# Kernel tuning notes

Measured on AMD Instinct MI355X. Metric: run time of the kernel, lower is better.

Reference implementation:

```python
import jax, jax.numpy as jnp
import numpy as np

B, T, S, E, H, V = 64, 32, 64, 128, 256, 32000


def setup_inputs() -> dict:
    key = jax.random.key(0)
    ks = jax.random.split(key, 13)
    n = lambda k, sh, s=1.0: jax.random.normal(k, sh, dtype=jnp.float32) * s
    return {
        "target": n(ks[0], (B, T, E)),
        "inp": n(ks[1], (B, T, E)),
        "pos_feature": n(ks[2], (B, E)),
        "encoder_state": n(ks[3], (B, H)),
        "encoder_output": n(ks[4], (B, S, 2 * H)),
        "W_ih": n(ks[5], (3 * H, 3 * E + H), 0.05),
        "W_hh": n(ks[6], (3 * H, H), 0.05),
        "b_ih": n(ks[7], (3 * H,), 0.05),
        "b_hh": n(ks[8], (3 * H,), 0.05),
        "Win_w": n(ks[9], (2 * H, H), 0.05),
        "Win_b": n(ks[10], (2 * H,), 0.05),
        "Wout_w": n(ks[11], (V, 3 * H), 0.05),
        "Wout_b": n(ks[12], (V,), 0.05),
    }


def reference(target, inp, pos_feature, encoder_state, encoder_output,
              W_ih, W_hh, b_ih, b_hh, Win_w, Win_b, Wout_w, Wout_b):
    bsz = target.shape[0]
    hdim = W_hh.shape[1]

    def gru_cell(x, h):
        gi = x @ W_ih.T + b_ih          # [B, 3H]
        gh = h @ W_hh.T + b_hh          # [B, 3H]
        i_r, i_z, i_n = jnp.split(gi, 3, axis=1)
        h_r, h_z, h_n = jnp.split(gh, 3, axis=1)
        r = jax.nn.sigmoid(i_r + h_r)
        z = jax.nn.sigmoid(i_z + h_z)
        n = jnp.tanh(i_n + r * h_n)
        return (1.0 - z) * n + z * h

    def step(hs, xs):
        dec_in, in_t = xs                                   # [B,E], [B,E]
        x = jnp.concatenate([dec_in, pos_feature, encoder_state, in_t], axis=1)
        hs = gru_cell(x, hs)
        q = hs @ Win_w.T + Win_b                            # [B, 2H]
        attn = jnp.einsum('bsd,bd->bs', encoder_output, q)  # [B, S]
        score = jax.nn.softmax(attn, axis=1)
        h_star = jnp.einsum('bs,bsd->bd', score, encoder_output)  # [B, 2H]
        feat = jnp.concatenate([h_star, hs], axis=1)        # [B, 3H]
        out = jax.nn.log_softmax(jax.nn.relu(feat @ Wout_w.T + Wout_b), axis=1)
        return hs, out

    hs0 = jnp.zeros((bsz, hdim), dtype=target.dtype)
    xs = (jnp.swapaxes(target, 0, 1), jnp.swapaxes(inp, 0, 1))  # time-major
    hs, outputs = jax.lax.scan(step, hs0, xs)
    return hs, outputs  # hs: [B,H], outputs: [T,B,V]
```

## Files before the change

kernel.cpp:

```cpp
#include <hip/hip_runtime.h>
#include <hip/hip_bf16.h>


typedef __attribute__((ext_vector_type(8))) short  s8v;
typedef __attribute__((ext_vector_type(8))) __bf16 bf8v;
typedef __attribute__((ext_vector_type(4))) float  f4v;
typedef __attribute__((ext_vector_type(2))) float  f2v;

#define DEV static __device__ __forceinline__

DEV ushort f2b(float f) {
  unsigned u = __float_as_uint(f);
  u += 0x7fffu + ((u >> 16) & 1u);
  return (ushort)(u >> 16);
}
DEV float b2fs(short s) { return __uint_as_float(((unsigned)(ushort)s) << 16); }

__global__ __launch_bounds__(256) void k_gather(
    const float* __restrict__ target, const float* __restrict__ inp,
    const float* __restrict__ posf,   const float* __restrict__ encs,
    ushort* __restrict__ X) {
  int tb = blockIdx.x; int t = tb >> 6, b = tb & 63;
  size_t xrow = (size_t)tb * 640;
  for (int c = threadIdx.x; c < 640; c += 256) {
    float v;
    if (c < 128)      v = target[((size_t)b * 32 + t) * 128 + c];
    else if (c < 256) v = posf[(size_t)b * 128 + (c - 128)];
    else if (c < 512) v = encs[(size_t)b * 256 + (c - 256)];
    else              v = inp[((size_t)b * 32 + t) * 128 + (c - 512)];
    X[xrow + c] = f2b(v);
  }
}

template <bool RELU>
__global__ __launch_bounds__(256) void k_gemm_bt(
    const ushort* __restrict__ A, const float* __restrict__ B,
    const float* __restrict__ bias, float* __restrict__ Out,
    int N, int K) {
  __shared__ __align__(16) ushort As[128 * 40];
  __shared__ __align__(16) ushort Bs[128 * 40];
  const int m0 = blockIdx.x * 128, n0 = blockIdx.y * 128;
  const int tid = threadIdx.x;
  const int lane = tid & 63, wv = tid >> 6;
  const int wm = (wv >> 1) * 64, wn = (wv & 1) * 64;
  const int fr = lane & 15, fq = lane >> 4;
  const int srow = tid >> 2, scol = (tid & 3) * 8;
  f4v acc[4][4];
#pragma unroll
  for (int i = 0; i < 4; ++i)
#pragma unroll
    for (int j = 0; j < 4; ++j) acc[i][j] = {0.f, 0.f, 0.f, 0.f};
  const ushort* ag = A + (size_t)(m0 + srow) * K + scol;
  const float*  bg = B + (size_t)(n0 + srow) * K + scol;
  for (int k0 = 0; k0 < K; k0 += 32) {
    s8v a0 = *(const s8v*)(ag + k0);
    s8v a1 = *(const s8v*)(ag + k0 + (size_t)64 * K);
    f4v b00 = *(const f4v*)(bg + k0);
    f4v b01 = *(const f4v*)(bg + k0 + 4);
    f4v b10 = *(const f4v*)(bg + k0 + (size_t)64 * K);
    f4v b11 = *(const f4v*)(bg + k0 + (size_t)64 * K + 4);
    s8v b0, b1;
#pragma unroll
    for (int u = 0; u < 4; ++u) {
      b0[u]     = (short)f2b(b00[u]);
      b0[u + 4] = (short)f2b(b01[u]);
      b1[u]     = (short)f2b(b10[u]);
      b1[u + 4] = (short)f2b(b11[u]);
    }
    __syncthreads();
    *(s8v*)&As[srow * 40 + scol] = a0;
    *(s8v*)&As[(srow + 64) * 40 + scol] = a1;
    *(s8v*)&Bs[srow * 40 + scol] = b0;
    *(s8v*)&Bs[(srow + 64) * 40 + scol] = b1;
    __syncthreads();
    bf8v af[4], bfr[4];
#pragma unroll
    for (int i = 0; i < 4; ++i)
      af[i] = *(const bf8v*)&As[(wm + i * 16 + fr) * 40 + fq * 8];
#pragma unroll
    for (int j = 0; j < 4; ++j)
      bfr[j] = *(const bf8v*)&Bs[(wn + j * 16 + fr) * 40 + fq * 8];
#pragma unroll
    for (int i = 0; i < 4; ++i)
#pragma unroll
      for (int j = 0; j < 4; ++j)
        acc[i][j] = __builtin_amdgcn_mfma_f32_16x16x32_bf16(af[i], bfr[j],
                                                            acc[i][j], 0, 0, 0);
  }
  float bj[4];
#pragma unroll
  for (int j = 0; j < 4; ++j) bj[j] = bias[n0 + wn + j * 16 + fr];
#pragma unroll
  for (int i = 0; i < 4; ++i) {
#pragma unroll
    for (int j = 0; j < 4; ++j) {
#pragma unroll
      for (int r = 0; r < 4; ++r) {
        int gm = m0 + wm + i * 16 + fq * 4 + r;
        int gn = n0 + wn + j * 16 + fr;
        float v = acc[i][j][r] + bj[j];
        if (RELU) v = fmaxf(v, 0.f);
        Out[(size_t)gm * N + gn] = v;
      }
    }
  }
}

__global__ __launch_bounds__(256) void k_recur(
    const float* __restrict__ gi_all,
    const float* __restrict__ eo,
    const float* __restrict__ Whh,
    const float* __restrict__ bhh,
    const float* __restrict__ Winw,
    const float* __restrict__ Winb,
    ushort* __restrict__ feat,
    float* __restrict__ hs_out) {
  const int b = blockIdx.x, t = threadIdx.x;
  __shared__ __align__(16) float h[256];
  __shared__ __align__(16) float q[512];
  __shared__ float attnp[64][4];
  __shared__ float score[64];
  const float* eoB = eo + (size_t)b * 32768;
  const float bhr = bhh[t], bhz = bhh[t + 256], bhn = bhh[t + 512];
  const float qb0 = Winb[t], qb1 = Winb[t + 256];
  const float* wr = Whh + t * 256;
  const float* wz = Whh + (t + 256) * 256;
  const float* wn = Whh + (t + 512) * 256;
  const float* w0 = Winw + t * 256;
  const float* w1 = Winw + (t + 256) * 256;
  h[t] = 0.f;
  __syncthreads();
  for (int st = 0; st < 32; ++st) {
    const float* gi = gi_all + ((size_t)st * 64 + b) * 768;
    float ar = bhr, az = bhz, an = bhn;
#pragma unroll 4
    for (int k = 0; k < 256; k += 8) {
      f4v ha = *(const f4v*)&h[k];
      f4v hb = *(const f4v*)&h[k + 4];
      f4v r0 = *(const f4v*)(wr + k), r1 = *(const f4v*)(wr + k + 4);
      f4v z0 = *(const f4v*)(wz + k), z1 = *(const f4v*)(wz + k + 4);
      f4v n0 = *(const f4v*)(wn + k), n1 = *(const f4v*)(wn + k + 4);
      float hv[8] = {ha.x, ha.y, ha.z, ha.w, hb.x, hb.y, hb.z, hb.w};
      float rv[8] = {r0.x, r0.y, r0.z, r0.w, r1.x, r1.y, r1.z, r1.w};
      float zv[8] = {z0.x, z0.y, z0.z, z0.w, z1.x, z1.y, z1.z, z1.w};
      float nv[8] = {n0.x, n0.y, n0.z, n0.w, n1.x, n1.y, n1.z, n1.w};
#pragma unroll
      for (int u = 0; u < 8; ++u) {
        ar = fmaf(hv[u], rv[u], ar);
        az = fmaf(hv[u], zv[u], az);
        an = fmaf(hv[u], nv[u], an);
      }
    }
    float r = 1.f / (1.f + __expf(-(gi[t] + ar)));
    float z = 1.f / (1.f + __expf(-(gi[t + 256] + az)));
    float e2 = __expf(2.f * (gi[t + 512] + r * an));
    float n = 1.f - 2.f / (e2 + 1.f);
    float hnew = (1.f - z) * n + z * h[t];
    __syncthreads();
    h[t] = hnew;
    __syncthreads();
    float a0 = qb0, a1 = qb1;
#pragma unroll 4
    for (int k = 0; k < 256; k += 8) {
      f4v ha = *(const f4v*)&h[k];
      f4v hb = *(const f4v*)&h[k + 4];
      f4v u00 = *(const f4v*)(w0 + k), u01 = *(const f4v*)(w0 + k + 4);
      f4v u10 = *(const f4v*)(w1 + k), u11 = *(const f4v*)(w1 + k + 4);
      float hv[8] = {ha.x, ha.y, ha.z, ha.w, hb.x, hb.y, hb.z, hb.w};
      float v0[8] = {u00.x, u00.y, u00.z, u00.w, u01.x, u01.y, u01.z, u01.w};
      float v1[8] = {u10.x, u10.y, u10.z, u10.w, u11.x, u11.y, u11.z, u11.w};
#pragma unroll
      for (int u = 0; u < 8; ++u) {
        a0 = fmaf(hv[u], v0[u], a0);
        a1 = fmaf(hv[u], v1[u], a1);
      }
    }
    q[t] = a0;
    q[t + 256] = a1;
    __syncthreads();
    {
      int s = t >> 2, p = t & 3;
      const float* ep = eoB + s * 512 + p * 128;
      const float* qp = &q[p * 128];
      float aa = 0.f;
#pragma unroll 4
      for (int dc = 0; dc < 128; dc += 8) {
        f4v e0 = *(const f4v*)(ep + dc), e1 = *(const f4v*)(ep + dc + 4);
        f4v q0 = *(const f4v*)(qp + dc), q1 = *(const f4v*)(qp + dc + 4);
        aa = fmaf(q0.x, e0.x, aa); aa = fmaf(q0.y, e0.y, aa);
        aa = fmaf(q0.z, e0.z, aa); aa = fmaf(q0.w, e0.w, aa);
        aa = fmaf(q1.x, e1.x, aa); aa = fmaf(q1.y, e1.y, aa);
        aa = fmaf(q1.z, e1.z, aa); aa = fmaf(q1.w, e1.w, aa);
      }
      attnp[s][p] = aa;
    }
    __syncthreads();
    if (t < 64) {
      float a = attnp[t][0] + attnp[t][1] + attnp[t][2] + attnp[t][3];
      float m = a;
#pragma unroll
      for (int off = 32; off > 0; off >>= 1) m = fmaxf(m, __shfl_xor(m, off));
      float e = __expf(a - m);
      float ss = e;
#pragma unroll
      for (int off = 32; off > 0; off >>= 1) ss += __shfl_xor(ss, off);
      score[t] = e / ss;
    }
    __syncthreads();
    {
      int d0 = 2 * t;
      float s0 = 0.f, s1 = 0.f;
#pragma unroll 8
      for (int s2 = 0; s2 < 64; ++s2) {
        float sc = score[s2];
        f2v ev = *(const f2v*)(eoB + s2 * 512 + d0);
        s0 = fmaf(sc, ev.x, s0);
        s1 = fmaf(sc, ev.y, s1);
      }
      size_t row = ((size_t)st * 64 + b) * 768;
      feat[row + d0] = f2b(s0);
      feat[row + d0 + 1] = f2b(s1);
      feat[row + 512 + t] = f2b(h[t]);
    }
    __syncthreads();
  }
  hs_out[(size_t)b * 256 + t] = h[t];
}

__global__ __launch_bounds__(256) void k_logsm(float* __restrict__ out) {
  float* p = out + (size_t)blockIdx.x * 32000;
  const int t = threadIdx.x;
  __shared__ float red[4];
  float m = 0.f;
  for (int c = t; c < 4000; c += 256) {
    f4v a = *(const f4v*)(p + (size_t)c * 8);
    f4v b = *(const f4v*)(p + (size_t)c * 8 + 4);
    m = fmaxf(m, fmaxf(fmaxf(a.x, a.y), fmaxf(a.z, a.w)));
    m = fmaxf(m, fmaxf(fmaxf(b.x, b.y), fmaxf(b.z, b.w)));
  }
#pragma unroll
  for (int off = 32; off > 0; off >>= 1) m = fmaxf(m, __shfl_xor(m, off));
  if ((t & 63) == 0) red[t >> 6] = m;
  __syncthreads();
  m = fmaxf(fmaxf(red[0], red[1]), fmaxf(red[2], red[3]));
  float s = 0.f;
  for (int c = t; c < 4000; c += 256) {
    f4v a = *(const f4v*)(p + (size_t)c * 8);
    f4v b = *(const f4v*)(p + (size_t)c * 8 + 4);
    s += __expf(a.x - m) + __expf(a.y - m) + __expf(a.z - m) + __expf(a.w - m);
    s += __expf(b.x - m) + __expf(b.y - m) + __expf(b.z - m) + __expf(b.w - m);
  }
#pragma unroll
  for (int off = 32; off > 0; off >>= 1) s += __shfl_xor(s, off);
  __syncthreads();
  if ((t & 63) == 0) red[t >> 6] = s;
  __syncthreads();
  s = red[0] + red[1] + red[2] + red[3];
  const float L = m + logf(s);
  for (int c = t; c < 4000; c += 256) {
    f4v a = *(const f4v*)(p + (size_t)c * 8);
    f4v b = *(const f4v*)(p + (size_t)c * 8 + 4);
    a.x -= L; a.y -= L; a.z -= L; a.w -= L;
    b.x -= L; b.y -= L; b.z -= L; b.w -= L;
    *(f4v*)(p + (size_t)c * 8) = a;
    *(f4v*)(p + (size_t)c * 8 + 4) = b;
  }
}

extern "C" void kernel_launch(void* const* d_in, const int* in_sizes, int n_in,
                              void* d_out, int out_size, void* d_ws, size_t ws_size,
                              hipStream_t stream) {
  (void)in_sizes; (void)n_in; (void)out_size; (void)ws_size;
  const float* target = (const float*)d_in[0];
  const float* inp    = (const float*)d_in[1];
  const float* posf   = (const float*)d_in[2];
  const float* encs   = (const float*)d_in[3];
  const float* enco   = (const float*)d_in[4];
  const float* Wih    = (const float*)d_in[5];
  const float* Whh    = (const float*)d_in[6];
  const float* bih    = (const float*)d_in[7];
  const float* bhh    = (const float*)d_in[8];
  const float* Winw   = (const float*)d_in[9];
  const float* Winb   = (const float*)d_in[10];
  const float* Woutw  = (const float*)d_in[11];
  const float* Woutb  = (const float*)d_in[12];

  char* ws = (char*)d_ws;
  ushort* X    = (ushort*)(ws);
  float*  gi   = (float*)(ws + 0x300000);
  ushort* feat = (ushort*)(ws + 0x900000);
  float* hs    = (float*)d_out;
  float* logits = hs + 16384;

  k_gather<<<2048, 256, 0, stream>>>(target, inp, posf, encs, X);
  k_gemm_bt<false><<<dim3(16, 6), 256, 0, stream>>>(X, Wih, bih, gi, 768, 640);
  k_recur<<<64, 256, 0, stream>>>(gi, enco, Whh, bhh, Winw, Winb, feat, hs);
  k_gemm_bt<true><<<dim3(16, 250), 256, 0, stream>>>(feat, Woutw, Woutb, logits,
                                                     32000, 768);
  k_logsm<<<2048, 256, 0, stream>>>(logits);
}
```

Before: 2.054 ms.

## Split GRU recurrence work across 1024 threads with shuffle reductions

The recurrent kernel now launches 1024 threads per block instead of 256. Each dot product (W_hh gates, query projection, attention scores, attention-weighted sum) is split across 2, 4 or 16 lanes and combined with cross-lane shuffle reductions. This shortens the serial per-thread loop in each of the 32 dependent time steps, which run on only 64 blocks and leave the GPU underused. The trailing per-step barrier is removed. The cost is extra shuffle and barrier work, many idle lanes in the gate and write phases, and higher register pressure at the larger block size.

Result: faster. 2.011 ms (-2.1%).

```diff
diff --git a/kernel.cpp b/kernel.cpp
--- a/kernel.cpp
+++ b/kernel.cpp
@@ -106,7 +106,7 @@
   }
 }
 
-__global__ __launch_bounds__(256) void k_recur(
+__global__ __launch_bounds__(1024) void k_recur(
     const float* __restrict__ gi_all,
     const float* __restrict__ eo,
     const float* __restrict__ Whh,
@@ -115,88 +115,91 @@
     const float* __restrict__ Winb,
     ushort* __restrict__ feat,
     float* __restrict__ hs_out) {
-  const int b = blockIdx.x, t = threadIdx.x;
+  const int b = blockIdx.x, tid = threadIdx.x;
   __shared__ __align__(16) float h[256];
   __shared__ __align__(16) float q[512];
-  __shared__ float attnp[64][4];
+  __shared__ float attnp[64];
   __shared__ float score[64];
   const float* eoB = eo + (size_t)b * 32768;
+
+  const int t = tid >> 2, p = tid & 3;
+  const float* wr = Whh + (size_t)t * 256 + p * 4;
+  const float* wz = wr + 65536;
+  const float* wn = wr + 131072;
   const float bhr = bhh[t], bhz = bhh[t + 256], bhn = bhh[t + 512];
-  const float qb0 = Winb[t], qb1 = Winb[t + 256];
-  const float* wr = Whh + t * 256;
-  const float* wz = Whh + (t + 256) * 256;
-  const float* wn = Whh + (t + 512) * 256;
-  const float* w0 = Winw + t * 256;
-  const float* w1 = Winw + (t + 256) * 256;
-  h[t] = 0.f;
+
+  const int qo = tid >> 1, qp = tid & 1;
+  const float* wq = Winw + (size_t)qo * 256 + qp * 4;
+  const float qb = Winb[qo];
+
+  const int as = tid >> 4, aj = tid & 15;
+
+  if (tid < 256) h[tid] = 0.f;
   __syncthreads();
+
   for (int st = 0; st < 32; ++st) {
     const float* gi = gi_all + ((size_t)st * 64 + b) * 768;
-    float ar = bhr, az = bhz, an = bhn;
-#pragma unroll 4
-    for (int k = 0; k < 256; k += 8) {
-      f4v ha = *(const f4v*)&h[k];
-      f4v hb = *(const f4v*)&h[k + 4];
-      f4v r0 = *(const f4v*)(wr + k), r1 = *(const f4v*)(wr + k + 4);
-      f4v z0 = *(const f4v*)(wz + k), z1 = *(const f4v*)(wz + k + 4);
-      f4v n0 = *(const f4v*)(wn + k), n1 = *(const f4v*)(wn + k + 4);
-      float hv[8] = {ha.x, ha.y, ha.z, ha.w, hb.x, hb.y, hb.z, hb.w};
-      float rv[8] = {r0.x, r0.y, r0.z, r0.w, r1.x, r1.y, r1.z, r1.w};
-      float zv[8] = {z0.x, z0.y, z0.z, z0.w, z1.x, z1.y, z1.z, z1.w};
-      float nv[8] = {n0.x, n0.y, n0.z, n0.w, n1.x, n1.y, n1.z, n1.w};
-#pragma unroll
-      for (int u = 0; u < 8; ++u) {
+    float g0 = gi[t], g1 = gi[t + 256], g2 = gi[t + 512];
+    float ar = 0.f, az = 0.f, an = 0.f;
+#pragma unroll
+    for (int i = 0; i < 16; ++i) {
+      f4v hv = *(const f4v*)&h[p * 4 + i * 16];
+      f4v rv = *(const f4v*)(wr + i * 16);
+      f4v zv = *(const f4v*)(wz + i * 16);
+      f4v nv = *(const f4v*)(wn + i * 16);
+#pragma unroll
+      for (int u = 0; u < 4; ++u) {
         ar = fmaf(hv[u], rv[u], ar);
         az = fmaf(hv[u], zv[u], az);
         an = fmaf(hv[u], nv[u], an);
       }
     }
-    float r = 1.f / (1.f + __expf(-(gi[t] + ar)));
-    float z = 1.f / (1.f + __expf(-(gi[t + 256] + az)));
-    float e2 = __expf(2.f * (gi[t + 512] + r * an));
-    float n = 1.f - 2.f / (e2 + 1.f);
-    float hnew = (1.f - z) * n + z * h[t];
-    __syncthreads();
-    h[t] = hnew;
-    __syncthreads();
-    float a0 = qb0, a1 = qb1;
-#pragma unroll 4
-    for (int k = 0; k < 256; k += 8) {
-      f4v ha = *(const f4v*)&h[k];
-      f4v hb = *(const f4v*)&h[k + 4];
-      f4v u00 = *(const f4v*)(w0 + k), u01 = *(const f4v*)(w0 + k + 4);
-      f4v u10 = *(const f4v*)(w1 + k), u11 = *(const f4v*)(w1 + k + 4);
-      float hv[8] = {ha.x, ha.y, ha.z, ha.w, hb.x, hb.y, hb.z, hb.w};
-      float v0[8] = {u00.x, u00.y, u00.z, u00.w, u01.x, u01.y, u01.z, u01.w};
-      float v1[8] = {u10.x, u10.y, u10.z, u10.w, u11.x, u11.y, u11.z, u11.w};
-#pragma unroll
-      for (int u = 0; u < 8; ++u) {
-        a0 = fmaf(hv[u], v0[u], a0);
-        a1 = fmaf(hv[u], v1[u], a1);
-      }
-    }
-    q[t] = a0;
-    q[t + 256] = a1;
-    __syncthreads();
-    {
-      int s = t >> 2, p = t & 3;
-      const float* ep = eoB + s * 512 + p * 128;
-      const float* qp = &q[p * 128];
-      float aa = 0.f;
-#pragma unroll 4
-      for (int dc = 0; dc < 128; dc += 8) {
-        f4v e0 = *(const f4v*)(ep + dc), e1 = *(const f4v*)(ep + dc + 4);
-        f4v q0 = *(const f4v*)(qp + dc), q1 = *(const f4v*)(qp + dc + 4);
-        aa = fmaf(q0.x, e0.x, aa); aa = fmaf(q0.y, e0.y, aa);
-        aa = fmaf(q0.z, e0.z, aa); aa = fmaf(q0.w, e0.w, aa);
-        aa = fmaf(q1.x, e1.x, aa); aa = fmaf(q1.y, e1.y, aa);
-        aa = fmaf(q1.z, e1.z, aa); aa = fmaf(q1.w, e1.w, aa);
-      }
-      attnp[s][p] = aa;
-    }
-    __syncthreads();
-    if (t < 64) {
-      float a = attnp[t][0] + attnp[t][1] + attnp[t][2] + attnp[t][3];
+    ar += __shfl_xor(ar, 1); ar += __shfl_xor(ar, 2);
+    az += __shfl_xor(az, 1); az += __shfl_xor(az, 2);
+    an += __shfl_xor(an, 1); an += __shfl_xor(an, 2);
+    float hnew = 0.f;
+    if (p == 0) {
+      float r = 1.f / (1.f + __expf(-(g0 + ar + bhr)));
+      float z = 1.f / (1.f + __expf(-(g1 + az + bhz)));
+      float e2 = __expf(2.f * (g2 + r * (an + bhn)));
+      float n = 1.f - 2.f / (e2 + 1.f);
+      hnew = (1.f - z) * n + z * h[t];
+    }
+    __syncthreads();
+    if (p == 0) h[t] = hnew;
+    __syncthreads();
+    float a0 = 0.f, a1 = 0.f;
+#pragma unroll
+    for (int i = 0; i < 32; i += 2) {
+      f4v h0 = *(const f4v*)&h[qp * 4 + i * 8];
+      f4v w0 = *(const f4v*)(wq + i * 8);
+      f4v h1 = *(const f4v*)&h[qp * 4 + i * 8 + 8];
+      f4v w1 = *(const f4v*)(wq + i * 8 + 8);
+#pragma unroll
+      for (int u = 0; u < 4; ++u) {
+        a0 = fmaf(h0[u], w0[u], a0);
+        a1 = fmaf(h1[u], w1[u], a1);
+      }
+    }
+    a0 += a1;
+    a0 += __shfl_xor(a0, 1);
+    if (qp == 0) q[qo] = a0 + qb;
+    __syncthreads();
+    float aa = 0.f;
+#pragma unroll
+    for (int i = 0; i < 8; ++i) {
+      int kk = aj * 4 + i * 64;
+      f4v ev = *(const f4v*)(eoB + (size_t)as * 512 + kk);
+      f4v qv = *(const f4v*)&q[kk];
+#pragma unroll
+      for (int u = 0; u < 4; ++u) aa = fmaf(ev[u], qv[u], aa);
+    }
+    aa += __shfl_xor(aa, 1); aa += __shfl_xor(aa, 2);
+    aa += __shfl_xor(aa, 4); aa += __shfl_xor(aa, 8);
+    if (aj == 0) attnp[as] = aa;
+    __syncthreads();
+    if (tid < 64) {
+      float a = attnp[tid];
       float m = a;
 #pragma unroll
       for (int off = 32; off > 0; off >>= 1) m = fmaxf(m, __shfl_xor(m, off));
@@ -204,27 +207,31 @@
       float ss = e;
 #pragma unroll
       for (int off = 32; off > 0; off >>= 1) ss += __shfl_xor(ss, off);
-      score[t] = e / ss;
-    }
-    __syncthreads();
+      score[tid] = e / ss;
+    }
+    __syncthreads();
+    size_t row = ((size_t)st * 64 + b) * 768;
     {
       int d0 = 2 * t;
       float s0 = 0.f, s1 = 0.f;
-#pragma unroll 8
-      for (int s2 = 0; s2 < 64; ++s2) {
+#pragma unroll
+      for (int i = 0; i < 16; ++i) {
+        int s2 = p * 16 + i;
         float sc = score[s2];
-        f2v ev = *(const f2v*)(eoB + s2 * 512 + d0);
+        f2v ev = *(const f2v*)(eoB + (size_t)s2 * 512 + d0);
         s0 = fmaf(sc, ev.x, s0);
         s1 = fmaf(sc, ev.y, s1);
       }
-      size_t row = ((size_t)st * 64 + b) * 768;
-      feat[row + d0] = f2b(s0);
-      feat[row + d0 + 1] = f2b(s1);
-      feat[row + 512 + t] = f2b(h[t]);
-    }
-    __syncthreads();
-  }
-  hs_out[(size_t)b * 256 + t] = h[t];
+      s0 += __shfl_xor(s0, 1); s0 += __shfl_xor(s0, 2);
+      s1 += __shfl_xor(s1, 1); s1 += __shfl_xor(s1, 2);
+      if (p == 0) {
+        feat[row + d0] = f2b(s0);
+        feat[row + d0 + 1] = f2b(s1);
+      }
+    }
+    if (tid < 256) feat[row + 512 + tid] = f2b(h[tid]);
+  }
+  if (tid < 256) hs_out[(size_t)b * 256 + tid] = h[tid];
 }
 
 __global__ __launch_bounds__(256) void k_logsm(float* __restrict__ out) {
@@ -294,7 +301,7 @@
 
   k_gather<<<2048, 256, 0, stream>>>(target, inp, posf, encs, X);
   k_gemm_bt<false><<<dim3(16, 6), 256, 0, stream>>>(X, Wih, bih, gi, 768, 640);
-  k_recur<<<64, 256, 0, stream>>>(gi, enco, Whh, bhh, Winw, Winb, feat, hs);
+  k_recur<<<64, 1024, 0, stream>>>(gi, enco, Whh, bhh, Winw, Winb, feat, hs);
   k_gemm_bt<true><<<dim3(16, 250), 256, 0, stream>>>(feat, Woutw, Woutb, logits,
                                                      32000, 768);
   k_logsm<<<2048, 256, 0, stream>>>(logits);
```
